# Performance work log

Hardware: AMD Instinct MI355X
Metric: run time of the kernel (lower is better)

Reference implementation:

```python
import jax, jax.numpy as jnp
import numpy as np

POOL = (2, 2)  # pool_size == strides, VALID padding


def setup_inputs() -> dict:
    key = jax.random.key(0)
    k1, k2 = jax.random.split(key)
    shape = (8, 512, 512, 32)  # B, H, W, C (NHWC, complex input as re/im pair)
    return {
        "x_real": jax.random.normal(k1, shape, dtype=jnp.float32),
        "x_imag": jax.random.normal(k2, shape, dtype=jnp.float32),
    }


def reference(x_real, x_imag):
    # Complex magnitude max-pool with argmax-based phase gather.
    # y = max_mag * exp(i * phase_at_argmax); returned as stacked (re, im).
    B, H, W, C = x_real.shape
    ph, pw = POOL
    Ho, Wo = H // ph, W // pw

    mag = jnp.sqrt(x_real * x_real + x_imag * x_imag)   # |x|
    phase = jnp.arctan2(x_imag, x_real)                 # angle(x)

    def windows(a):
        # [B,H,W,C] -> [B,Ho,Wo,C,ph*pw]  (non-overlapping pooling windows)
        return (a.reshape(B, Ho, ph, Wo, pw, C)
                 .transpose(0, 1, 3, 5, 2, 4)
                 .reshape(B, Ho, Wo, C, ph * pw))

    mag_w = windows(mag)
    idx = jnp.argmax(mag_w, axis=-1)                    # [B,Ho,Wo,C]
    y_mag = jnp.take_along_axis(mag_w, idx[..., None], axis=-1)[..., 0]
    y_phase = jnp.take_along_axis(windows(phase), idx[..., None], axis=-1)[..., 0]

    # y = y_mag * exp(1j * y_phase), returned as [B,Ho,Wo,C,2] (re, im)
    return jnp.stack([y_mag * jnp.cos(y_phase), y_mag * jnp.sin(y_phase)], axis=-1)
```

## Files before the change

kernel.cpp:

```cpp
#include <hip/hip_runtime.h>


typedef float f32x4 __attribute__((ext_vector_type(4)));

constexpr int B  = 8;
constexpr int H  = 512;
constexpr int W  = 512;
constexpr int C  = 32;
constexpr int Ho = H / 2;
constexpr int Wo = W / 2;
constexpr long TOTAL = (long)B * Ho * Wo * (C / 4);
constexpr int  BLOCK = 256;
constexpr int  GRID  = 2048;
constexpr int  ITERS = (int)(TOTAL / ((long)BLOCK * GRID));
static_assert((long)BLOCK * GRID * ITERS == TOTAL, "exact tiling");

__device__ __forceinline__ float ref_mag(float r, float i) {
  return __fsqrt_rn(__fadd_rn(__fmul_rn(r, r), __fmul_rn(i, i)));
}

struct Frag { f32x4 R[4], I[4]; };

__device__ __forceinline__ void load_frag(const float* __restrict__ xr,
                                          const float* __restrict__ xi,
                                          long g, Frag& f) {
  const int c4 = (int)(g & 7);
  long t = g >> 3;
  const int wo = (int)(t & (Wo - 1));   t >>= 8;
  const int ho = (int)(t & (Ho - 1));   t >>= 8;
  const int b  = (int)t;
  const long ibase = ((((long)b * H + 2 * ho) * W) + 2 * wo) * C + c4 * 4;
  const long rs = (long)W * C;
  f.R[0] = *(const f32x4*)(xr + ibase);
  f.R[1] = *(const f32x4*)(xr + ibase + C);
  f.R[2] = *(const f32x4*)(xr + ibase + rs);
  f.R[3] = *(const f32x4*)(xr + ibase + rs + C);
  f.I[0] = *(const f32x4*)(xi + ibase);
  f.I[1] = *(const f32x4*)(xi + ibase + C);
  f.I[2] = *(const f32x4*)(xi + ibase + rs);
  f.I[3] = *(const f32x4*)(xi + ibase + rs + C);
}

__device__ __forceinline__ void compute_store(float* __restrict__ out,
                                              long g, const Frag& f) {
  const int c4 = (int)(g & 7);
  long t = g >> 3;
  const int wo = (int)(t & (Wo - 1));   t >>= 8;
  const int ho = (int)(t & (Ho - 1));   t >>= 8;
  const int b  = (int)t;

  float ore[4], oim[4];
#pragma unroll
  for (int j = 0; j < 4; ++j) {
    float br = f.R[0][j];
    float bi = f.I[0][j];
    float bm = ref_mag(br, bi);
#pragma unroll
    for (int k = 1; k < 4; ++k) {
      const float rr = f.R[k][j];
      const float ii = f.I[k][j];
      const float m  = ref_mag(rr, ii);
      if (m > bm) { bm = m; br = rr; bi = ii; }
    }
    ore[j] = br;
    oim[j] = bi;
  }

  const long obase = ((((long)b * Ho + ho) * Wo + wo) * C + c4 * 4) * 2;
  f32x4 o0, o1;
  o0.x = ore[0]; o0.y = oim[0]; o0.z = ore[1]; o0.w = oim[1];
  o1.x = ore[2]; o1.y = oim[2]; o1.z = ore[3]; o1.w = oim[3];
  *(f32x4*)(out + obase)     = o0;
  *(f32x4*)(out + obase + 4) = o1;
}

__global__ __launch_bounds__(BLOCK) void cmaxpool_kernel(
    const float* __restrict__ xr,
    const float* __restrict__ xi,
    float* __restrict__ out) {
  const long stride = (long)GRID * BLOCK;
  long g = (long)blockIdx.x * BLOCK + threadIdx.x;

  Frag fa, fb;
  load_frag(xr, xi, g, fa);
#pragma unroll
  for (int it = 0; it < ITERS; it += 2) {
    if (it + 1 < ITERS) load_frag(xr, xi, g + stride, fb);
    __builtin_amdgcn_sched_barrier(0);
    compute_store(out, g, fa);
    if (it + 2 < ITERS) load_frag(xr, xi, g + 2 * stride, fa);
    __builtin_amdgcn_sched_barrier(0);
    if (it + 1 < ITERS) compute_store(out, g + stride, fb);
    g += 2 * stride;
  }
}

extern "C" void kernel_launch(void* const* d_in, const int* in_sizes, int n_in,
                              void* d_out, int out_size, void* d_ws, size_t ws_size,
                              hipStream_t stream) {
  const float* xr = (const float*)d_in[0];
  const float* xi = (const float*)d_in[1];
  float* out = (float*)d_out;
  cmaxpool_kernel<<<GRID, BLOCK, 0, stream>>>(xr, xi, out);
}
```

Before: 128.5 us.

## Split each pooling window across lane pairs and reduce columns with shuffles

Each thread now loads one input column (two rows) of 4 channels instead of a full 2x2 window, and the horizontal max is finished by exchanging partial results with the partner lane through shuffles. Each lane writes half of the output vector. This doubles the thread count and makes adjacent lanes read contiguous memory along W, which should improve load coalescing and memory-level parallelism. The cost is extra shuffle instructions, tie-breaking logic kept consistent with the reference argmax order, and narrower per-thread stores.

```diff
diff --git a/kernel.cpp b/kernel.cpp
--- a/kernel.cpp
+++ b/kernel.cpp
@@ -9,7 +9,7 @@
 constexpr int C  = 32;
 constexpr int Ho = H / 2;
 constexpr int Wo = W / 2;
-constexpr long TOTAL = (long)B * Ho * Wo * (C / 4);
+constexpr long TOTAL = (long)B * Ho * W * (C / 4);
 constexpr int  BLOCK = 256;
 constexpr int  GRID  = 2048;
 constexpr int  ITERS = (int)(TOTAL / ((long)BLOCK * GRID));
@@ -19,59 +19,78 @@
   return __fsqrt_rn(__fadd_rn(__fmul_rn(r, r), __fmul_rn(i, i)));
 }
 
-struct Frag { f32x4 R[4], I[4]; };
+struct Frag { f32x4 r0, r1, i0, i1; };
 
 __device__ __forceinline__ void load_frag(const float* __restrict__ xr,
                                           const float* __restrict__ xi,
                                           long g, Frag& f) {
   const int c4 = (int)(g & 7);
-  long t = g >> 3;
-  const int wo = (int)(t & (Wo - 1));   t >>= 8;
-  const int ho = (int)(t & (Ho - 1));   t >>= 8;
-  const int b  = (int)t;
-  const long ibase = ((((long)b * H + 2 * ho) * W) + 2 * wo) * C + c4 * 4;
-  const long rs = (long)W * C;
-  f.R[0] = *(const f32x4*)(xr + ibase);
-  f.R[1] = *(const f32x4*)(xr + ibase + C);
-  f.R[2] = *(const f32x4*)(xr + ibase + rs);
-  f.R[3] = *(const f32x4*)(xr + ibase + rs + C);
-  f.I[0] = *(const f32x4*)(xi + ibase);
-  f.I[1] = *(const f32x4*)(xi + ibase + C);
-  f.I[2] = *(const f32x4*)(xi + ibase + rs);
-  f.I[3] = *(const f32x4*)(xi + ibase + rs + C);
+  const int w  = (int)((g >> 3) & (W - 1));
+  const int ho = (int)((g >> 12) & (Ho - 1));
+  const int b  = (int)(g >> 20);
+  const long base0 = (((long)(b * H + 2 * ho) * W) + w) * C + c4 * 4;
+  const long base1 = base0 + (long)W * C;
+  f.r0 = *(const f32x4*)(xr + base0);
+  f.r1 = *(const f32x4*)(xr + base1);
+  f.i0 = *(const f32x4*)(xi + base0);
+  f.i1 = *(const f32x4*)(xi + base1);
 }
 
 __device__ __forceinline__ void compute_store(float* __restrict__ out,
                                               long g, const Frag& f) {
   const int c4 = (int)(g & 7);
-  long t = g >> 3;
-  const int wo = (int)(t & (Wo - 1));   t >>= 8;
-  const int ho = (int)(t & (Ho - 1));   t >>= 8;
-  const int b  = (int)t;
+  const int w  = (int)((g >> 3) & (W - 1));
+  const int ho = (int)((g >> 12) & (Ho - 1));
+  const int b  = (int)(g >> 20);
+  const int parity = w & 1;
+  const int wo = w >> 1;
 
-  float ore[4], oim[4];
+  float vm[4], vre[4], vim[4];
+  int vrow = 0;
 #pragma unroll
   for (int j = 0; j < 4; ++j) {
-    float br = f.R[0][j];
-    float bi = f.I[0][j];
-    float bm = ref_mag(br, bi);
-#pragma unroll
-    for (int k = 1; k < 4; ++k) {
-      const float rr = f.R[k][j];
-      const float ii = f.I[k][j];
-      const float m  = ref_mag(rr, ii);
-      if (m > bm) { bm = m; br = rr; bi = ii; }
-    }
-    ore[j] = br;
-    oim[j] = bi;
+    const float m0 = ref_mag(f.r0[j], f.i0[j]);
+    const float m1 = ref_mag(f.r1[j], f.i1[j]);
+    const bool p1 = (m1 > m0);
+    vm[j]  = p1 ? m1 : m0;
+    vre[j] = p1 ? f.r1[j] : f.r0[j];
+    vim[j] = p1 ? f.i1[j] : f.i0[j];
+    vrow  |= (int)p1 << j;
   }
 
-  const long obase = ((((long)b * Ho + ho) * Wo + wo) * C + c4 * 4) * 2;
-  f32x4 o0, o1;
-  o0.x = ore[0]; o0.y = oim[0]; o0.z = ore[1]; o0.w = oim[1];
-  o1.x = ore[2]; o1.y = oim[2]; o1.z = ore[3]; o1.w = oim[3];
-  *(f32x4*)(out + obase)     = o0;
-  *(f32x4*)(out + obase + 4) = o1;
+  float pm[4], pre[4], pim[4];
+#pragma unroll
+  for (int j = 0; j < 4; ++j) {
+    pm[j]  = __shfl_xor(vm[j], 8);
+    pre[j] = __shfl_xor(vre[j], 8);
+    pim[j] = __shfl_xor(vim[j], 8);
+  }
+  const int prow = __shfl_xor(vrow, 8);
+
+  float fre[4], fim[4];
+#pragma unroll
+  for (int j = 0; j < 4; ++j) {
+    const float Em  = parity ? pm[j]  : vm[j];
+    const float Ere = parity ? pre[j] : vre[j];
+    const float Eim = parity ? pim[j] : vim[j];
+    const int   Er  = (parity ? prow : vrow) >> j & 1;
+    const float Om  = parity ? vm[j]  : pm[j];
+    const float Ore = parity ? vre[j] : pre[j];
+    const float Oim = parity ? vim[j] : pim[j];
+    const int   Or  = (parity ? vrow : prow) >> j & 1;
+    const bool chooseO = (Om > Em) || ((Om == Em) && Er && !Or);
+    fre[j] = chooseO ? Ore : Ere;
+    fim[j] = chooseO ? Oim : Eim;
+  }
+
+  const long obase =
+      ((((long)(b * Ho + ho) * Wo) + wo) * C + c4 * 4) * 2 + parity * 4;
+  f32x4 o;
+  o.x = parity ? fre[2] : fre[0];
+  o.y = parity ? fim[2] : fim[0];
+  o.z = parity ? fre[3] : fre[1];
+  o.w = parity ? fim[3] : fim[1];
+  *(f32x4*)(out + obase) = o;
 }
 
 __global__ __launch_bounds__(BLOCK) void cmaxpool_kernel(
```

Result: no change. 130.8 us (+1.8%).
